# Kernel tuning notes

Hardware: AMD Instinct MI355X
Metric: run time of the kernel (lower is better)

The kernel has to match this reference:

```python
import jax, jax.numpy as jnp
import numpy as np

N_NODES = 50000
N_EDGES = 800000
D_FEAT = 96
PROMPT_DIM = 96


def setup_inputs() -> dict:
    key = jax.random.key(0)
    k1, k2, k3, k4 = jax.random.split(key, 4)
    graph_embedding = jax.random.normal(k1, (N_NODES, D_FEAT), dtype=jnp.float32)
    weight = jax.random.normal(k2, (1, PROMPT_DIM), dtype=jnp.float32)
    src = jax.random.randint(k3, (N_EDGES,), 0, N_NODES, dtype=jnp.int64)
    dst = jax.random.randint(k4, (N_EDGES,), 0, N_NODES, dtype=jnp.int64)
    return {"graph_embedding": graph_embedding, "weight": weight,
            "src": src, "dst": dst, "num_nodes": N_NODES}


def reference(graph_embedding, weight, src, dst, num_nodes):
    # message on edge e: concat(ft[src[e]], weight)  -> [E, D_FEAT + PROMPT_DIM]
    # reduce: sum of messages over incoming edges of each dst node.
    # Feature half: scatter-sum of gathered src features.
    agg_ft = jax.ops.segment_sum(graph_embedding[src], dst, num_segments=num_nodes)
    # Prompt half: identical prompt on every edge => in_degree[v] * weight.
    ones = jnp.ones((src.shape[0],), dtype=graph_embedding.dtype)
    in_deg = jax.ops.segment_sum(ones, dst, num_segments=num_nodes)  # [N]
    agg_p = in_deg[:, None] * weight  # [N, PROMPT_DIM] (weight broadcasts from [1,P])
    return jnp.concatenate([agg_ft, agg_p], axis=1)
```

## Files before the change

kernel.cpp:

```cpp
#include <hip/hip_runtime.h>

#define D_FEAT 96
#define P_DIM 96
#define OUT_DIM 192
#define SCAN_BLK 256
#define NODES_PER_BLK 8
#define LPN 24
#define LPNB 12
#define NPBB 16
#define RNG_SHIFT 8
#define RNG_NODES 256
#define NBLK_A 1024
#define FS_CAP 6144

typedef float f32x4 __attribute__((ext_vector_type(4)));
typedef unsigned int u32;
typedef u32 u32x4 __attribute__((ext_vector_type(4)));

__global__ __launch_bounds__(256) void zero_k(float* __restrict__ out,
                                              float* __restrict__ deg,
                                              int n_out, int n_deg) {
    int stride = gridDim.x * blockDim.x;
    for (int i = blockIdx.x * blockDim.x + threadIdx.x; i < n_out; i += stride)
        out[i] = 0.0f;
    for (int i = blockIdx.x * blockDim.x + threadIdx.x; i < n_deg; i += stride)
        deg[i] = 0.0f;
}

__global__ __launch_bounds__(256) void degf_k(const int* __restrict__ dst,
                                              float* __restrict__ deg,
                                              int n_edges) {
    int e = blockIdx.x * blockDim.x + threadIdx.x;
    if (e < n_edges) atomicAdd(deg + dst[e], 1.0f);
}

__global__ __launch_bounds__(256) void scatter_k(const float* __restrict__ emb,
                                                 const int* __restrict__ src,
                                                 const int* __restrict__ dst,
                                                 float* __restrict__ out,
                                                 int n_edges) {
    int idx = blockIdx.x * blockDim.x + threadIdx.x;
    int e = idx / D_FEAT;
    if (e >= n_edges) return;
    int c = idx - e * D_FEAT;
    atomicAdd(out + (size_t)dst[e] * OUT_DIM + c, emb[(size_t)src[e] * D_FEAT + c]);
}

__global__ __launch_bounds__(256) void prompt_k(const float* __restrict__ w,
                                                const float* __restrict__ deg,
                                                float* __restrict__ out,
                                                int n_nodes) {
    int idx = blockIdx.x * blockDim.x + threadIdx.x;
    if (idx >= n_nodes * P_DIM) return;
    int v = idx / P_DIM;
    int c = idx - v * P_DIM;
    out[(size_t)v * OUT_DIM + P_DIM + c] = deg[v] * w[c];
}


__device__ __forceinline__ u32 f2bf_rn(float f) {
    u32 b = __float_as_uint(f);
    return (b + 0x7fffu + ((b >> 16) & 1u)) >> 16;
}


__global__ __launch_bounds__(256) void conv_hist_k(
        const f32x4* __restrict__ emb4, u32x4* __restrict__ embb, int n8, int do_conv,
        const int* __restrict__ dst, int* __restrict__ cnt,
        int n_edges, int nr, int chunk) {
    int b = blockIdx.x, t = threadIdx.x;
    if (do_conv) {
        int gs = gridDim.x * 256;
        for (int i = b * 256 + t; i < n8; i += gs) {
            f32x4 a = emb4[2 * i];
            f32x4 c = emb4[2 * i + 1];
            u32x4 o;
            o.x = f2bf_rn(a.x) | (f2bf_rn(a.y) << 16);
            o.y = f2bf_rn(a.z) | (f2bf_rn(a.w) << 16);
            o.z = f2bf_rn(c.x) | (f2bf_rn(c.y) << 16);
            o.w = f2bf_rn(c.z) | (f2bf_rn(c.w) << 16);
            embb[i] = o;
        }
    }
    __shared__ int h[RNG_NODES];
    h[t] = 0;
    __syncthreads();
    int beg = b * chunk;
    int end = beg + chunk; if (end > n_edges) end = n_edges;
    for (int i = beg + t; i < end; i += 256)
        atomicAdd(&h[dst[i] >> RNG_SHIFT], 1);
    __syncthreads();
    if (t < nr) cnt[t * NBLK_A + b] = h[t];
}

__global__ __launch_bounds__(SCAN_BLK) void scan4_k(int* __restrict__ cnt,
                                                    int* __restrict__ aux) {
    __shared__ int buf[SCAN_BLK];
    int t = threadIdx.x;
    int base = blockIdx.x * (SCAN_BLK * 4) + t * 4;
    int v0 = cnt[base], v1 = cnt[base + 1], v2 = cnt[base + 2], v3 = cnt[base + 3];
    int s = v0 + v1 + v2 + v3;
    buf[t] = s;
    __syncthreads();
    for (int off = 1; off < SCAN_BLK; off <<= 1) {
        int x = (t >= off) ? buf[t - off] : 0;
        __syncthreads();
        buf[t] += x;
        __syncthreads();
    }
    int ex = buf[t] - s;
    cnt[base]     = ex;
    cnt[base + 1] = ex + v0;
    cnt[base + 2] = ex + v0 + v1;
    cnt[base + 3] = ex + v0 + v1 + v2;
    if (t == SCAN_BLK - 1) aux[blockIdx.x] = buf[t];
}

__global__ __launch_bounds__(256) void binwrite_k(const int* __restrict__ src,
                                                  const int* __restrict__ dst,
                                                  const int* __restrict__ cnt,
                                                  const int* __restrict__ aux,
                                                  int* __restrict__ pack,
                                                  int n_edges, int nr, int chunk) {
    __shared__ int buf[SCAN_BLK];
    __shared__ int cur[RNG_NODES];
    int b = blockIdx.x, t = threadIdx.x;
    int av = (t < nr) ? aux[t] : 0;
    buf[t] = av;
    __syncthreads();
    for (int off = 1; off < SCAN_BLK; off <<= 1) {
        int x = (t >= off) ? buf[t - off] : 0;
        __syncthreads();
        buf[t] += x;
        __syncthreads();
    }
    if (t < nr) cur[t] = (buf[t] - av) + cnt[t * NBLK_A + b];
    __syncthreads();
    int beg = b * chunk;
    int end = beg + chunk; if (end > n_edges) end = n_edges;
    for (int i = beg + t; i < end; i += 256) {
        int d = dst[i];
        int pos = atomicAdd(&cur[d >> RNG_SHIFT], 1);
        pack[pos] = (src[i] << RNG_SHIFT) | (d & (RNG_NODES - 1));
    }
}

__global__ __launch_bounds__(256) void finesort_k(const int* __restrict__ aux,
                                                  const int* __restrict__ pack,
                                                  int* __restrict__ offs,
                                                  int* __restrict__ sorted_src,
                                                  int n_nodes, int n_edges, int nr) {
    __shared__ int buf[SCAN_BLK];
    __shared__ int h[RNG_NODES];
    __shared__ int cur[RNG_NODES];
    __shared__ int win[FS_CAP];
    int r = blockIdx.x, t = threadIdx.x;
    int av = (t < nr) ? aux[t] : 0;
    buf[t] = av;
    __syncthreads();
    for (int off = 1; off < SCAN_BLK; off <<= 1) {
        int x = (t >= off) ? buf[t - off] : 0;
        __syncthreads();
        buf[t] += x;
        __syncthreads();
    }
    int start = buf[r] - aux[r];
    int end = buf[r];
    int wlen = end - start;
    bool fits = (wlen <= FS_CAP);

    h[t] = 0;
    __syncthreads();
    if (fits) {
        for (int i = t; i < wlen; i += 256) {
            int p = pack[start + i];
            win[i] = p;
            atomicAdd(&h[p & (RNG_NODES - 1)], 1);
        }
    } else {
        for (int i = start + t; i < end; i += 256)
            atomicAdd(&h[pack[i] & (RNG_NODES - 1)], 1);
    }
    __syncthreads();
    int v = h[t];
    for (int off = 1; off < RNG_NODES; off <<= 1) {
        int x = (t >= off) ? h[t - off] : 0;
        __syncthreads();
        h[t] += x;
        __syncthreads();
    }
    int o = start + h[t] - v;
    int node = (r << RNG_SHIFT) + t;
    if (node < n_nodes) offs[node] = o;
    cur[t] = o;
    __syncthreads();
    if (fits) {
        for (int i = t; i < wlen; i += 256) {
            int p = win[i];
            int pos = atomicAdd(&cur[p & (RNG_NODES - 1)], 1);
            sorted_src[pos] = p >> RNG_SHIFT;
        }
    } else {
        for (int i = start + t; i < end; i += 256) {
            int p = pack[i];
            int pos = atomicAdd(&cur[p & (RNG_NODES - 1)], 1);
            sorted_src[pos] = p >> RNG_SHIFT;
        }
    }
}


#define ACC8(A, g)                                                        \
    {                                                                     \
        A[0] += __uint_as_float((g).x << 16);                             \
        A[1] += __uint_as_float((g).x & 0xffff0000u);                     \
        A[2] += __uint_as_float((g).y << 16);                             \
        A[3] += __uint_as_float((g).y & 0xffff0000u);                     \
        A[4] += __uint_as_float((g).z << 16);                             \
        A[5] += __uint_as_float((g).z & 0xffff0000u);                     \
        A[6] += __uint_as_float((g).w << 16);                             \
        A[7] += __uint_as_float((g).w & 0xffff0000u);                     \
    }

__global__ __launch_bounds__(NPBB * LPNB) void aggb_k(
        const u32x4* __restrict__ embb,
        const float* __restrict__ w,
        const int* __restrict__ offs,
        const int* __restrict__ sorted_src,
        float* __restrict__ out, int n_nodes, int n_edges) {
    int t = threadIdx.x;
    int sub = t / LPNB;
    int lane = t - sub * LPNB;
    int node = blockIdx.x * NPBB + sub;
    if (node >= n_nodes) return;

    int start = offs[node];
    int endp = (node + 1 < n_nodes) ? offs[node + 1] : n_edges;
    int cnt = endp - start;
    const int* sp = sorted_src + start;

    float aA[8] = {0.f, 0.f, 0.f, 0.f, 0.f, 0.f, 0.f, 0.f};
    float aB[8] = {0.f, 0.f, 0.f, 0.f, 0.f, 0.f, 0.f, 0.f};
    int j = 0;
    if (cnt >= 8) {
        int s0 = sp[0], s1 = sp[1], s2 = sp[2], s3 = sp[3];
        for (; j + 7 < cnt; j += 4) {
            int t0 = sp[j + 4], t1 = sp[j + 5], t2 = sp[j + 6], t3 = sp[j + 7];
            u32x4 g0 = embb[(size_t)s0 * LPNB + lane];
            u32x4 g1 = embb[(size_t)s1 * LPNB + lane];
            u32x4 g2 = embb[(size_t)s2 * LPNB + lane];
            u32x4 g3 = embb[(size_t)s3 * LPNB + lane];
            ACC8(aA, g0); ACC8(aB, g1); ACC8(aA, g2); ACC8(aB, g3);
            s0 = t0; s1 = t1; s2 = t2; s3 = t3;
        }
        u32x4 g0 = embb[(size_t)s0 * LPNB + lane];
        u32x4 g1 = embb[(size_t)s1 * LPNB + lane];
        u32x4 g2 = embb[(size_t)s2 * LPNB + lane];
        u32x4 g3 = embb[(size_t)s3 * LPNB + lane];
        ACC8(aA, g0); ACC8(aB, g1); ACC8(aA, g2); ACC8(aB, g3);
        j += 4;
    }
    for (; j + 3 < cnt; j += 4) {
        int s0 = sp[j], s1 = sp[j + 1], s2 = sp[j + 2], s3 = sp[j + 3];
        u32x4 g0 = embb[(size_t)s0 * LPNB + lane];
        u32x4 g1 = embb[(size_t)s1 * LPNB + lane];
        u32x4 g2 = embb[(size_t)s2 * LPNB + lane];
        u32x4 g3 = embb[(size_t)s3 * LPNB + lane];
        ACC8(aA, g0); ACC8(aB, g1); ACC8(aA, g2); ACC8(aB, g3);
    }
    for (; j < cnt; ++j) {
        u32x4 g0 = embb[(size_t)sp[j] * LPNB + lane];
        ACC8(aA, g0);
    }

    f32x4 lo = {aA[0] + aB[0], aA[1] + aB[1], aA[2] + aB[2], aA[3] + aB[3]};
    f32x4 hi = {aA[4] + aB[4], aA[5] + aB[5], aA[6] + aB[6], aA[7] + aB[7]};

    f32x4* outrow = (f32x4*)(out + (size_t)node * OUT_DIM);
    const f32x4* w4 = (const f32x4*)w;
    float c = (float)cnt;
    f32x4 plo = c * w4[lane * 2];
    f32x4 phi = c * w4[lane * 2 + 1];
    __builtin_nontemporal_store(lo, outrow + lane * 2);
    __builtin_nontemporal_store(hi, outrow + lane * 2 + 1);
    __builtin_nontemporal_store(plo, outrow + 24 + lane * 2);
    __builtin_nontemporal_store(phi, outrow + 24 + lane * 2 + 1);
}

__global__ __launch_bounds__(NODES_PER_BLK * LPN) void agg4p_k(
        const f32x4* __restrict__ emb4,
        const f32x4* __restrict__ w4,
        const int* __restrict__ offs,
        const int* __restrict__ sorted_src,
        float* __restrict__ out, int n_nodes, int n_edges) {
    int t = threadIdx.x;
    int sub = t / LPN;
    int lane = t - sub * LPN;
    int node = blockIdx.x * NODES_PER_BLK + sub;
    if (node >= n_nodes) return;

    int start = offs[node];
    int endp = (node + 1 < n_nodes) ? offs[node + 1] : n_edges;
    int cnt = endp - start;
    const int* sp = sorted_src + start;

    f32x4 a0 = {0.f, 0.f, 0.f, 0.f};
    f32x4 a1 = a0, a2 = a0, a3 = a0;
    int j = 0;
    if (cnt >= 8) {
        int s0 = sp[0], s1 = sp[1], s2 = sp[2], s3 = sp[3];
        for (; j + 7 < cnt; j += 4) {
            int t0 = sp[j + 4], t1 = sp[j + 5], t2 = sp[j + 6], t3 = sp[j + 7];
            f32x4 v0 = emb4[(size_t)s0 * LPN + lane];
            f32x4 v1 = emb4[(size_t)s1 * LPN + lane];
            f32x4 v2 = emb4[(size_t)s2 * LPN + lane];
            f32x4 v3 = emb4[(size_t)s3 * LPN + lane];
            a0 += v0; a1 += v1; a2 += v2; a3 += v3;
            s0 = t0; s1 = t1; s2 = t2; s3 = t3;
        }
        f32x4 v0 = emb4[(size_t)s0 * LPN + lane];
        f32x4 v1 = emb4[(size_t)s1 * LPN + lane];
        f32x4 v2 = emb4[(size_t)s2 * LPN + lane];
        f32x4 v3 = emb4[(size_t)s3 * LPN + lane];
        a0 += v0; a1 += v1; a2 += v2; a3 += v3;
        j += 4;
    }
    for (; j + 3 < cnt; j += 4) {
        int s0 = sp[j], s1 = sp[j + 1], s2 = sp[j + 2], s3 = sp[j + 3];
        f32x4 v0 = emb4[(size_t)s0 * LPN + lane];
        f32x4 v1 = emb4[(size_t)s1 * LPN + lane];
        f32x4 v2 = emb4[(size_t)s2 * LPN + lane];
        f32x4 v3 = emb4[(size_t)s3 * LPN + lane];
        a0 += v0; a1 += v1; a2 += v2; a3 += v3;
    }
    for (; j < cnt; ++j) {
        a0 += emb4[(size_t)sp[j] * LPN + lane];
    }
    f32x4 ft = (a0 + a1) + (a2 + a3);

    f32x4* outrow = (f32x4*)(out + (size_t)node * OUT_DIM);
    float c = (float)cnt;
    f32x4 pv = c * w4[lane];
    __builtin_nontemporal_store(ft, outrow + lane);
    __builtin_nontemporal_store(pv, outrow + LPN + lane);
}

extern "C" void kernel_launch(void* const* d_in, const int* in_sizes, int n_in,
                              void* d_out, int out_size, void* d_ws, size_t ws_size,
                              hipStream_t stream) {
    const float* emb = (const float*)d_in[0];
    const float* w   = (const float*)d_in[1];
    const int*   src = (const int*)d_in[2];
    const int*   dst = (const int*)d_in[3];
    float* out = (float*)d_out;

    const int n_nodes = in_sizes[0] / D_FEAT;
    const int n_edges = in_sizes[2];
    const int nr = (n_nodes + RNG_NODES - 1) >> RNG_SHIFT;
    const int cnt_len = nr * NBLK_A;
    const int chunk = (n_edges + NBLK_A - 1) / NBLK_A;

    size_t base_ints = (size_t)cnt_len + SCAN_BLK + n_nodes + 2 * (size_t)n_edges;
    size_t embb_off  = (base_ints + 3) & ~(size_t)3;
    size_t need_f32  = base_ints * sizeof(int);
    size_t need_bf16 = (embb_off + (size_t)n_nodes * 48) * sizeof(int);
    bool ok = (nr <= SCAN_BLK) &&
              (n_nodes <= (1 << (31 - RNG_SHIFT - 1)));

    if (ws_size < need_f32 || !ok) {
        float* deg = (float*)d_ws;
        int n_out = n_nodes * OUT_DIM;
        int blocks = (n_out + 255) / 256;
        if (blocks > 2048) blocks = 2048;
        zero_k<<<blocks, 256, 0, stream>>>(out, deg, n_out, n_nodes);
        degf_k<<<(n_edges + 255) / 256, 256, 0, stream>>>(dst, deg, n_edges);
        long long total = (long long)n_edges * D_FEAT;
        scatter_k<<<(int)((total + 255) / 256), 256, 0, stream>>>(emb, src, dst, out, n_edges);
        prompt_k<<<(n_nodes * P_DIM + 255) / 256, 256, 0, stream>>>(w, deg, out, n_nodes);
        return;
    }

    int* cnt        = (int*)d_ws;
    int* aux        = cnt + cnt_len;
    int* offs       = aux + SCAN_BLK;
    int* pack       = offs + n_nodes;
    int* sorted_src = pack + n_edges;
    u32x4* embb     = (u32x4*)((int*)d_ws + embb_off);

    bool use_bf16 = (ws_size >= need_bf16);
    int n8 = n_nodes * LPNB;

    conv_hist_k<<<NBLK_A, 256, 0, stream>>>((const f32x4*)emb, embb, n8,
                                            use_bf16 ? 1 : 0, dst, cnt,
                                            n_edges, nr, chunk);
    scan4_k<<<nr, SCAN_BLK, 0, stream>>>(cnt, aux);
    binwrite_k<<<NBLK_A, 256, 0, stream>>>(src, dst, cnt, aux, pack, n_edges, nr, chunk);
    finesort_k<<<nr, 256, 0, stream>>>(aux, pack, offs, sorted_src, n_nodes, n_edges, nr);
    if (use_bf16) {
        aggb_k<<<(n_nodes + NPBB - 1) / NPBB, NPBB * LPNB, 0, stream>>>(
            embb, w, offs, sorted_src, out, n_nodes, n_edges);
    } else {
        agg4p_k<<<(n_nodes + NODES_PER_BLK - 1) / NODES_PER_BLK, NODES_PER_BLK * LPN, 0, stream>>>(
            (const f32x4*)emb, (const f32x4*)w, offs, sorted_src, out, n_nodes, n_edges);
    }
}
```

Before: 65.85 us.

## Gather FP8-quantized embeddings and enlarge sort-phase thread blocks

Adds an FP8 mode, chosen by default when the builtins exist and the workspace is large enough. The conversion pass packs each 96-float embedding row into 96 bytes, and a new aggregation kernel decodes those bytes with packed FP8-to-f32 conversions. This halves the bytes read by the random per-edge gathers compared with the bf16 path. The histogram, bin-write and fine-sort kernels now run with 1024-thread blocks and 256 partition blocks, and the count scan becomes a simple per-block scan. FP8 e4m3 quantization adds much larger rounding error than bf16, which risks failing accuracy tolerances.

```diff
diff --git a/kernel.cpp b/kernel.cpp
--- a/kernel.cpp
+++ b/kernel.cpp
@@ -6,16 +6,25 @@
 #define SCAN_BLK 256
 #define NODES_PER_BLK 8
 #define LPN 24
-#define LPNB 12
-#define NPBB 16
 #define RNG_SHIFT 8
 #define RNG_NODES 256
-#define NBLK_A 1024
+#define NBLK_A 256
+#define BIG_T 1024
 #define FS_CAP 6144
 
 typedef float f32x4 __attribute__((ext_vector_type(4)));
+typedef float f32x2 __attribute__((ext_vector_type(2)));
 typedef unsigned int u32;
 typedef u32 u32x4 __attribute__((ext_vector_type(4)));
+
+#if defined(__has_builtin)
+#if __has_builtin(__builtin_amdgcn_cvt_pk_f32_fp8) && __has_builtin(__builtin_amdgcn_cvt_pk_fp8_f32)
+#define HAVE_FP8 1
+#endif
+#endif
+#ifndef HAVE_FP8
+#define HAVE_FP8 0
+#endif
 
 __global__ __launch_bounds__(256) void zero_k(float* __restrict__ out,
                                               float* __restrict__ deg,
@@ -63,15 +72,25 @@
     return (b + 0x7fffu + ((b >> 16) & 1u)) >> 16;
 }
 
-
-__global__ __launch_bounds__(256) void conv_hist_k(
-        const f32x4* __restrict__ emb4, u32x4* __restrict__ embb, int n8, int do_conv,
+#if HAVE_FP8
+__device__ __forceinline__ u32 enc4_fp8(float a, float b, float c, float d) {
+    u32 r = __builtin_amdgcn_cvt_pk_fp8_f32(a, b, 0u, false);
+    r = __builtin_amdgcn_cvt_pk_fp8_f32(c, d, r, true);
+    return r;
+}
+#endif
+
+
+__global__ __launch_bounds__(BIG_T) void conv_hist_k(
+        const f32x4* __restrict__ emb4, u32x4* __restrict__ embq,
+        int nq, int mode,
         const int* __restrict__ dst, int* __restrict__ cnt,
         int n_edges, int nr, int chunk) {
     int b = blockIdx.x, t = threadIdx.x;
-    if (do_conv) {
-        int gs = gridDim.x * 256;
-        for (int i = b * 256 + t; i < n8; i += gs) {
+    int gs = gridDim.x * BIG_T;
+    int gid = b * BIG_T + t;
+    if (mode == 1) {
+        for (int i = gid; i < nq; i += gs) {
             f32x4 a = emb4[2 * i];
             f32x4 c = emb4[2 * i + 1];
             u32x4 o;
@@ -79,28 +98,43 @@
             o.y = f2bf_rn(a.z) | (f2bf_rn(a.w) << 16);
             o.z = f2bf_rn(c.x) | (f2bf_rn(c.y) << 16);
             o.w = f2bf_rn(c.z) | (f2bf_rn(c.w) << 16);
-            embb[i] = o;
-        }
-    }
+            embq[i] = o;
+        }
+    }
+#if HAVE_FP8
+    else if (mode == 2) {
+        for (int i = gid; i < nq; i += gs) {
+            f32x4 a = emb4[4 * i];
+            f32x4 b4 = emb4[4 * i + 1];
+            f32x4 c = emb4[4 * i + 2];
+            f32x4 d = emb4[4 * i + 3];
+            u32x4 o;
+            o.x = enc4_fp8(a.x, a.y, a.z, a.w);
+            o.y = enc4_fp8(b4.x, b4.y, b4.z, b4.w);
+            o.z = enc4_fp8(c.x, c.y, c.z, c.w);
+            o.w = enc4_fp8(d.x, d.y, d.z, d.w);
+            embq[i] = o;
+        }
+    }
+#endif
     __shared__ int h[RNG_NODES];
-    h[t] = 0;
+    if (t < RNG_NODES) h[t] = 0;
     __syncthreads();
     int beg = b * chunk;
     int end = beg + chunk; if (end > n_edges) end = n_edges;
-    for (int i = beg + t; i < end; i += 256)
+    for (int i = beg + t; i < end; i += BIG_T)
         atomicAdd(&h[dst[i] >> RNG_SHIFT], 1);
     __syncthreads();
     if (t < nr) cnt[t * NBLK_A + b] = h[t];
 }
 
-__global__ __launch_bounds__(SCAN_BLK) void scan4_k(int* __restrict__ cnt,
-                                                    int* __restrict__ aux) {
+__global__ __launch_bounds__(SCAN_BLK) void scan_block_k(int* __restrict__ cnt,
+                                                         int* __restrict__ aux, int n) {
     __shared__ int buf[SCAN_BLK];
     int t = threadIdx.x;
-    int base = blockIdx.x * (SCAN_BLK * 4) + t * 4;
-    int v0 = cnt[base], v1 = cnt[base + 1], v2 = cnt[base + 2], v3 = cnt[base + 3];
-    int s = v0 + v1 + v2 + v3;
-    buf[t] = s;
+    int i = blockIdx.x * SCAN_BLK + t;
+    int v = (i < n) ? cnt[i] : 0;
+    buf[t] = v;
     __syncthreads();
     for (int off = 1; off < SCAN_BLK; off <<= 1) {
         int x = (t >= off) ? buf[t - off] : 0;
@@ -108,106 +142,194 @@
         buf[t] += x;
         __syncthreads();
     }
-    int ex = buf[t] - s;
-    cnt[base]     = ex;
-    cnt[base + 1] = ex + v0;
-    cnt[base + 2] = ex + v0 + v1;
-    cnt[base + 3] = ex + v0 + v1 + v2;
+    if (i < n) cnt[i] = buf[t] - v;
     if (t == SCAN_BLK - 1) aux[blockIdx.x] = buf[t];
 }
 
-__global__ __launch_bounds__(256) void binwrite_k(const int* __restrict__ src,
-                                                  const int* __restrict__ dst,
-                                                  const int* __restrict__ cnt,
-                                                  const int* __restrict__ aux,
-                                                  int* __restrict__ pack,
-                                                  int n_edges, int nr, int chunk) {
+__global__ __launch_bounds__(BIG_T) void binwrite_k(const int* __restrict__ src,
+                                                    const int* __restrict__ dst,
+                                                    const int* __restrict__ cnt,
+                                                    const int* __restrict__ aux,
+                                                    int* __restrict__ pack,
+                                                    int n_edges, int nr, int chunk) {
     __shared__ int buf[SCAN_BLK];
     __shared__ int cur[RNG_NODES];
     int b = blockIdx.x, t = threadIdx.x;
-    int av = (t < nr) ? aux[t] : 0;
-    buf[t] = av;
+    int av = 0;
+    if (t < SCAN_BLK) { av = (t < nr) ? aux[t] : 0; buf[t] = av; }
     __syncthreads();
     for (int off = 1; off < SCAN_BLK; off <<= 1) {
-        int x = (t >= off) ? buf[t - off] : 0;
-        __syncthreads();
-        buf[t] += x;
+        int x = 0;
+        if (t < SCAN_BLK && t >= off) x = buf[t - off];
+        __syncthreads();
+        if (t < SCAN_BLK) buf[t] += x;
         __syncthreads();
     }
     if (t < nr) cur[t] = (buf[t] - av) + cnt[t * NBLK_A + b];
     __syncthreads();
     int beg = b * chunk;
     int end = beg + chunk; if (end > n_edges) end = n_edges;
-    for (int i = beg + t; i < end; i += 256) {
+    for (int i = beg + t; i < end; i += BIG_T) {
         int d = dst[i];
         int pos = atomicAdd(&cur[d >> RNG_SHIFT], 1);
         pack[pos] = (src[i] << RNG_SHIFT) | (d & (RNG_NODES - 1));
     }
 }
 
-__global__ __launch_bounds__(256) void finesort_k(const int* __restrict__ aux,
-                                                  const int* __restrict__ pack,
-                                                  int* __restrict__ offs,
-                                                  int* __restrict__ sorted_src,
-                                                  int n_nodes, int n_edges, int nr) {
+__global__ __launch_bounds__(BIG_T) void finesort_k(const int* __restrict__ aux,
+                                                    const int* __restrict__ pack,
+                                                    int* __restrict__ offs,
+                                                    int* __restrict__ sorted_src,
+                                                    int n_nodes, int n_edges, int nr) {
     __shared__ int buf[SCAN_BLK];
     __shared__ int h[RNG_NODES];
     __shared__ int cur[RNG_NODES];
     __shared__ int win[FS_CAP];
     int r = blockIdx.x, t = threadIdx.x;
-    int av = (t < nr) ? aux[t] : 0;
-    buf[t] = av;
+    int av = 0;
+    if (t < SCAN_BLK) { av = (t < nr) ? aux[t] : 0; buf[t] = av; }
     __syncthreads();
     for (int off = 1; off < SCAN_BLK; off <<= 1) {
-        int x = (t >= off) ? buf[t - off] : 0;
-        __syncthreads();
-        buf[t] += x;
+        int x = 0;
+        if (t < SCAN_BLK && t >= off) x = buf[t - off];
+        __syncthreads();
+        if (t < SCAN_BLK) buf[t] += x;
         __syncthreads();
     }
     int start = buf[r] - aux[r];
     int end = buf[r];
     int wlen = end - start;
     bool fits = (wlen <= FS_CAP);
-
-    h[t] = 0;
+    if (t < RNG_NODES) h[t] = 0;
     __syncthreads();
     if (fits) {
-        for (int i = t; i < wlen; i += 256) {
+        for (int i = t; i < wlen; i += BIG_T) {
             int p = pack[start + i];
             win[i] = p;
             atomicAdd(&h[p & (RNG_NODES - 1)], 1);
         }
     } else {
-        for (int i = start + t; i < end; i += 256)
+        for (int i = start + t; i < end; i += BIG_T)
             atomicAdd(&h[pack[i] & (RNG_NODES - 1)], 1);
     }
     __syncthreads();
-    int v = h[t];
+    int v = (t < RNG_NODES) ? h[t] : 0;
     for (int off = 1; off < RNG_NODES; off <<= 1) {
-        int x = (t >= off) ? h[t - off] : 0;
-        __syncthreads();
-        h[t] += x;
-        __syncthreads();
-    }
-    int o = start + h[t] - v;
-    int node = (r << RNG_SHIFT) + t;
-    if (node < n_nodes) offs[node] = o;
-    cur[t] = o;
+        int x = 0;
+        if (t < RNG_NODES && t >= off) x = h[t - off];
+        __syncthreads();
+        if (t < RNG_NODES) h[t] += x;
+        __syncthreads();
+    }
+    if (t < RNG_NODES) {
+        int o = start + h[t] - v;
+        int node = (r << RNG_SHIFT) + t;
+        if (node < n_nodes) offs[node] = o;
+        cur[t] = o;
+    }
     __syncthreads();
     if (fits) {
-        for (int i = t; i < wlen; i += 256) {
+        for (int i = t; i < wlen; i += BIG_T) {
             int p = win[i];
             int pos = atomicAdd(&cur[p & (RNG_NODES - 1)], 1);
             sorted_src[pos] = p >> RNG_SHIFT;
         }
     } else {
-        for (int i = start + t; i < end; i += 256) {
+        for (int i = start + t; i < end; i += BIG_T) {
             int p = pack[i];
             int pos = atomicAdd(&cur[p & (RNG_NODES - 1)], 1);
             sorted_src[pos] = p >> RNG_SHIFT;
         }
     }
 }
+
+
+#if HAVE_FP8
+#define DEC16(A, g)                                                         \
+    {                                                                       \
+        A[0] += __builtin_amdgcn_cvt_pk_f32_fp8((g).x, false);              \
+        A[1] += __builtin_amdgcn_cvt_pk_f32_fp8((g).x, true);               \
+        A[2] += __builtin_amdgcn_cvt_pk_f32_fp8((g).y, false);              \
+        A[3] += __builtin_amdgcn_cvt_pk_f32_fp8((g).y, true);               \
+        A[4] += __builtin_amdgcn_cvt_pk_f32_fp8((g).z, false);              \
+        A[5] += __builtin_amdgcn_cvt_pk_f32_fp8((g).z, true);               \
+        A[6] += __builtin_amdgcn_cvt_pk_f32_fp8((g).w, false);              \
+        A[7] += __builtin_amdgcn_cvt_pk_f32_fp8((g).w, true);               \
+    }
+
+__global__ __launch_bounds__(192) void aggf8_k(
+        const u32x4* __restrict__ emb8,
+        const float* __restrict__ w,
+        const int* __restrict__ offs,
+        const int* __restrict__ sorted_src,
+        float* __restrict__ out, int n_nodes, int n_edges) {
+    int t = threadIdx.x;
+    int sub = t / 6;
+    int lane = t - sub * 6;
+    int node = blockIdx.x * 32 + sub;
+    if (node >= n_nodes) return;
+
+    int start = offs[node];
+    int endp = (node + 1 < n_nodes) ? offs[node + 1] : n_edges;
+    int cnt = endp - start;
+    const int* sp = sorted_src + start;
+
+    f32x2 A[8];
+    #pragma unroll
+    for (int k = 0; k < 8; ++k) A[k] = (f32x2){0.f, 0.f};
+
+    int j = 0;
+    if (cnt >= 8) {
+        int s0 = sp[0], s1 = sp[1], s2 = sp[2], s3 = sp[3];
+        for (; j + 7 < cnt; j += 4) {
+            int t0 = sp[j + 4], t1 = sp[j + 5], t2 = sp[j + 6], t3 = sp[j + 7];
+            u32x4 g0 = emb8[(size_t)s0 * 6 + lane];
+            u32x4 g1 = emb8[(size_t)s1 * 6 + lane];
+            u32x4 g2 = emb8[(size_t)s2 * 6 + lane];
+            u32x4 g3 = emb8[(size_t)s3 * 6 + lane];
+            DEC16(A, g0); DEC16(A, g1); DEC16(A, g2); DEC16(A, g3);
+            s0 = t0; s1 = t1; s2 = t2; s3 = t3;
+        }
+        u32x4 g0 = emb8[(size_t)s0 * 6 + lane];
+        u32x4 g1 = emb8[(size_t)s1 * 6 + lane];
+        u32x4 g2 = emb8[(size_t)s2 * 6 + lane];
+        u32x4 g3 = emb8[(size_t)s3 * 6 + lane];
+        DEC16(A, g0); DEC16(A, g1); DEC16(A, g2); DEC16(A, g3);
+        j += 4;
+    }
+    for (; j + 3 < cnt; j += 4) {
+        int s0 = sp[j], s1 = sp[j + 1], s2 = sp[j + 2], s3 = sp[j + 3];
+        u32x4 g0 = emb8[(size_t)s0 * 6 + lane];
+        u32x4 g1 = emb8[(size_t)s1 * 6 + lane];
+        u32x4 g2 = emb8[(size_t)s2 * 6 + lane];
+        u32x4 g3 = emb8[(size_t)s3 * 6 + lane];
+        DEC16(A, g0); DEC16(A, g1); DEC16(A, g2); DEC16(A, g3);
+    }
+    for (; j < cnt; ++j) {
+        u32x4 g0 = emb8[(size_t)sp[j] * 6 + lane];
+        DEC16(A, g0);
+    }
+
+    f32x4 o0 = {A[0].x, A[0].y, A[1].x, A[1].y};
+    f32x4 o1 = {A[2].x, A[2].y, A[3].x, A[3].y};
+    f32x4 o2 = {A[4].x, A[4].y, A[5].x, A[5].y};
+    f32x4 o3 = {A[6].x, A[6].y, A[7].x, A[7].y};
+
+    f32x4* outrow = (f32x4*)(out + (size_t)node * OUT_DIM);
+    const f32x4* w4 = (const f32x4*)w;
+    float c = (float)cnt;
+    int q = lane * 4;
+    __builtin_nontemporal_store(o0, outrow + q);
+    __builtin_nontemporal_store(o1, outrow + q + 1);
+    __builtin_nontemporal_store(o2, outrow + q + 2);
+    __builtin_nontemporal_store(o3, outrow + q + 3);
+    f32x4 p0 = c * w4[q], p1 = c * w4[q + 1], p2 = c * w4[q + 2], p3 = c * w4[q + 3];
+    __builtin_nontemporal_store(p0, outrow + 24 + q);
+    __builtin_nontemporal_store(p1, outrow + 24 + q + 1);
+    __builtin_nontemporal_store(p2, outrow + 24 + q + 2);
+    __builtin_nontemporal_store(p3, outrow + 24 + q + 3);
+}
+#endif
 
 
 #define ACC8(A, g)                                                        \
@@ -222,16 +344,16 @@
         A[7] += __uint_as_float((g).w & 0xffff0000u);                     \
     }
 
-__global__ __launch_bounds__(NPBB * LPNB) void aggb_k(
+__global__ __launch_bounds__(192) void aggb_k(
         const u32x4* __restrict__ embb,
         const float* __restrict__ w,
         const int* __restrict__ offs,
         const int* __restrict__ sorted_src,
         float* __restrict__ out, int n_nodes, int n_edges) {
     int t = threadIdx.x;
-    int sub = t / LPNB;
-    int lane = t - sub * LPNB;
-    int node = blockIdx.x * NPBB + sub;
+    int sub = t / 12;
+    int lane = t - sub * 12;
+    int node = blockIdx.x * 16 + sub;
     if (node >= n_nodes) return;
 
     int start = offs[node];
@@ -246,30 +368,30 @@
         int s0 = sp[0], s1 = sp[1], s2 = sp[2], s3 = sp[3];
         for (; j + 7 < cnt; j += 4) {
             int t0 = sp[j + 4], t1 = sp[j + 5], t2 = sp[j + 6], t3 = sp[j + 7];
-            u32x4 g0 = embb[(size_t)s0 * LPNB + lane];
-            u32x4 g1 = embb[(size_t)s1 * LPNB + lane];
-            u32x4 g2 = embb[(size_t)s2 * LPNB + lane];
-            u32x4 g3 = embb[(size_t)s3 * LPNB + lane];
+            u32x4 g0 = embb[(size_t)s0 * 12 + lane];
+            u32x4 g1 = embb[(size_t)s1 * 12 + lane];
+            u32x4 g2 = embb[(size_t)s2 * 12 + lane];
+            u32x4 g3 = embb[(size_t)s3 * 12 + lane];
             ACC8(aA, g0); ACC8(aB, g1); ACC8(aA, g2); ACC8(aB, g3);
             s0 = t0; s1 = t1; s2 = t2; s3 = t3;
         }
-        u32x4 g0 = embb[(size_t)s0 * LPNB + lane];
-        u32x4 g1 = embb[(size_t)s1 * LPNB + lane];
-        u32x4 g2 = embb[(size_t)s2 * LPNB + lane];
-        u32x4 g3 = embb[(size_t)s3 * LPNB + lane];
+        u32x4 g0 = embb[(size_t)s0 * 12 + lane];
+        u32x4 g1 = embb[(size_t)s1 * 12 + lane];
+        u32x4 g2 = embb[(size_t)s2 * 12 + lane];
+        u32x4 g3 = embb[(size_t)s3 * 12 + lane];
         ACC8(aA, g0); ACC8(aB, g1); ACC8(aA, g2); ACC8(aB, g3);
         j += 4;
     }
     for (; j + 3 < cnt; j += 4) {
         int s0 = sp[j], s1 = sp[j + 1], s2 = sp[j + 2], s3 = sp[j + 3];
-        u32x4 g0 = embb[(size_t)s0 * LPNB + lane];
-        u32x4 g1 = embb[(size_t)s1 * LPNB + lane];
-        u32x4 g2 = embb[(size_t)s2 * LPNB + lane];
-        u32x4 g3 = embb[(size_t)s3 * LPNB + lane];
+        u32x4 g0 = embb[(size_t)s0 * 12 + lane];
+        u32x4 g1 = embb[(size_t)s1 * 12 + lane];
+        u32x4 g2 = embb[(size_t)s2 * 12 + lane];
+        u32x4 g3 = embb[(size_t)s3 * 12 + lane];
         ACC8(aA, g0); ACC8(aB, g1); ACC8(aA, g2); ACC8(aB, g3);
     }
     for (; j < cnt; ++j) {
-        u32x4 g0 = embb[(size_t)sp[j] * LPNB + lane];
+        u32x4 g0 = embb[(size_t)sp[j] * 12 + lane];
         ACC8(aA, g0);
     }
 
@@ -307,24 +429,6 @@
     f32x4 a0 = {0.f, 0.f, 0.f, 0.f};
     f32x4 a1 = a0, a2 = a0, a3 = a0;
     int j = 0;
-    if (cnt >= 8) {
-        int s0 = sp[0], s1 = sp[1], s2 = sp[2], s3 = sp[3];
-        for (; j + 7 < cnt; j += 4) {
-            int t0 = sp[j + 4], t1 = sp[j + 5], t2 = sp[j + 6], t3 = sp[j + 7];
-            f32x4 v0 = emb4[(size_t)s0 * LPN + lane];
-            f32x4 v1 = emb4[(size_t)s1 * LPN + lane];
-            f32x4 v2 = emb4[(size_t)s2 * LPN + lane];
-            f32x4 v3 = emb4[(size_t)s3 * LPN + lane];
-            a0 += v0; a1 += v1; a2 += v2; a3 += v3;
-            s0 = t0; s1 = t1; s2 = t2; s3 = t3;
-        }
-        f32x4 v0 = emb4[(size_t)s0 * LPN + lane];
-        f32x4 v1 = emb4[(size_t)s1 * LPN + lane];
-        f32x4 v2 = emb4[(size_t)s2 * LPN + lane];
-        f32x4 v3 = emb4[(size_t)s3 * LPN + lane];
-        a0 += v0; a1 += v1; a2 += v2; a3 += v3;
-        j += 4;
-    }
     for (; j + 3 < cnt; j += 4) {
         int s0 = sp[j], s1 = sp[j + 1], s2 = sp[j + 2], s3 = sp[j + 3];
         f32x4 v0 = emb4[(size_t)s0 * LPN + lane];
@@ -358,13 +462,15 @@
     const int n_edges = in_sizes[2];
     const int nr = (n_nodes + RNG_NODES - 1) >> RNG_SHIFT;
     const int cnt_len = nr * NBLK_A;
+    const int nb_cnt = (cnt_len + SCAN_BLK - 1) / SCAN_BLK;
     const int chunk = (n_edges + NBLK_A - 1) / NBLK_A;
 
     size_t base_ints = (size_t)cnt_len + SCAN_BLK + n_nodes + 2 * (size_t)n_edges;
-    size_t embb_off  = (base_ints + 3) & ~(size_t)3;
+    size_t embq_off  = (base_ints + 3) & ~(size_t)3;
     size_t need_f32  = base_ints * sizeof(int);
-    size_t need_bf16 = (embb_off + (size_t)n_nodes * 48) * sizeof(int);
-    bool ok = (nr <= SCAN_BLK) &&
+    size_t need_bf16 = (embq_off + (size_t)n_nodes * 48) * sizeof(int);
+    size_t need_fp8  = (embq_off + (size_t)n_nodes * 24) * sizeof(int);
+    bool ok = (nr <= SCAN_BLK) && (nb_cnt <= SCAN_BLK) &&
               (n_nodes <= (1 << (31 - RNG_SHIFT - 1)));
 
     if (ws_size < need_f32 || !ok) {
@@ -385,20 +491,31 @@
     int* offs       = aux + SCAN_BLK;
     int* pack       = offs + n_nodes;
     int* sorted_src = pack + n_edges;
-    u32x4* embb     = (u32x4*)((int*)d_ws + embb_off);
-
-    bool use_bf16 = (ws_size >= need_bf16);
-    int n8 = n_nodes * LPNB;
-
-    conv_hist_k<<<NBLK_A, 256, 0, stream>>>((const f32x4*)emb, embb, n8,
-                                            use_bf16 ? 1 : 0, dst, cnt,
-                                            n_edges, nr, chunk);
-    scan4_k<<<nr, SCAN_BLK, 0, stream>>>(cnt, aux);
-    binwrite_k<<<NBLK_A, 256, 0, stream>>>(src, dst, cnt, aux, pack, n_edges, nr, chunk);
-    finesort_k<<<nr, 256, 0, stream>>>(aux, pack, offs, sorted_src, n_nodes, n_edges, nr);
-    if (use_bf16) {
-        aggb_k<<<(n_nodes + NPBB - 1) / NPBB, NPBB * LPNB, 0, stream>>>(
-            embb, w, offs, sorted_src, out, n_nodes, n_edges);
+    u32x4* embq     = (u32x4*)((int*)d_ws + embq_off);
+
+    int mode = 0;
+    int nq = 0;
+#if HAVE_FP8
+    if (ws_size >= need_fp8) { mode = 2; nq = n_nodes * 6; }
+    else if (ws_size >= need_bf16) { mode = 1; nq = n_nodes * 12; }
+#else
+    if (ws_size >= need_bf16) { mode = 1; nq = n_nodes * 12; }
+#endif
+
+    conv_hist_k<<<NBLK_A, BIG_T, 0, stream>>>((const f32x4*)emb, embq, nq, mode,
+                                              dst, cnt, n_edges, nr, chunk);
+    scan_block_k<<<nb_cnt, SCAN_BLK, 0, stream>>>(cnt, aux, cnt_len);
+    binwrite_k<<<NBLK_A, BIG_T, 0, stream>>>(src, dst, cnt, aux, pack, n_edges, nr, chunk);
+    finesort_k<<<nr, BIG_T, 0, stream>>>(aux, pack, offs, sorted_src, n_nodes, n_edges, nr);
+#if HAVE_FP8
+    if (mode == 2) {
+        aggf8_k<<<(n_nodes + 31) / 32, 192, 0, stream>>>(
+            embq, w, offs, sorted_src, out, n_nodes, n_edges);
+    } else
+#endif
+    if (mode == 1) {
+        aggb_k<<<(n_nodes + 15) / 16, 192, 0, stream>>>(
+            embq, w, offs, sorted_src, out, n_nodes, n_edges);
     } else {
         agg4p_k<<<(n_nodes + NODES_PER_BLK - 1) / NODES_PER_BLK, NODES_PER_BLK * LPN, 0, stream>>>(
             (const f32x4*)emb, (const f32x4*)w, offs, sorted_src, out, n_nodes, n_edges);
```

Result: faster. 60.55 us (-8.0%).
